# Kernel optimization log

Hardware: AMD Instinct MI355X
Metric: run time of the kernel (lower is better)

Reference implementation:

```python
import jax, jax.numpy as jnp
import numpy as np

D_MODEL = 1024
N_HEADS = 16
HEAD_DIM = D_MODEL // N_HEADS
SEQ = 2048
BATCH = 2
ROPE_BASE = 10000.0


def rope_cos_sin(seq_len, dim, dtype=jnp.float32):
    inv_freq = 1.0 / (ROPE_BASE ** (jnp.arange(0, dim, 2, dtype=jnp.float32) / dim))
    pos = jnp.arange(seq_len, dtype=jnp.float32)
    freqs = jnp.outer(pos, inv_freq)              # [S, dim/2]
    emb = jnp.concatenate([freqs, freqs], axis=-1)  # [S, dim]
    return jnp.cos(emb).astype(dtype), jnp.sin(emb).astype(dtype)


def rotate_half(x):
    x1, x2 = jnp.split(x, 2, axis=-1)
    return jnp.concatenate([-x2, x1], axis=-1)


def setup_inputs() -> dict:
    key = jax.random.key(0)
    kx, kq, kk, kv, ko = jax.random.split(key, 5)
    x = jax.random.normal(kx, (BATCH, SEQ, D_MODEL), dtype=jnp.float32)
    # causal boolean mask, broadcastable to [B, H, S, S]
    attn_mask = jnp.tril(jnp.ones((SEQ, SEQ), dtype=bool))[None, None]
    s = 1.0 / np.sqrt(D_MODEL)
    Wq = jax.random.normal(kq, (D_MODEL, D_MODEL), dtype=jnp.float32) * s
    Wk = jax.random.normal(kk, (D_MODEL, D_MODEL), dtype=jnp.float32) * s
    Wv = jax.random.normal(kv, (D_MODEL, D_MODEL), dtype=jnp.float32) * s
    Wo = jax.random.normal(ko, (D_MODEL, D_MODEL), dtype=jnp.float32) * s
    return {"x": x, "attn_mask": attn_mask, "Wq": Wq, "Wk": Wk, "Wv": Wv, "Wo": Wo}


def reference(x, attn_mask, Wq, Wk, Wv, Wo):
    B, S, _ = x.shape
    dtype = x.dtype
    # projections (nn.Linear: x @ W.T)
    def split_heads(t):
        return t.reshape(B, S, N_HEADS, HEAD_DIM).transpose(0, 2, 1, 3)  # [B,H,S,Dh]
    q = split_heads(x @ Wq.T)
    k = split_heads(x @ Wk.T)
    v = split_heads(x @ Wv.T)
    # RoPE
    cos, sin = rope_cos_sin(S, HEAD_DIM, dtype)  # [S, Dh]
    cos = cos[None, None]
    sin = sin[None, None]
    q = q * cos + rotate_half(q) * sin
    k = k * cos + rotate_half(k) * sin
    # float mask: 0 where True, finfo.min where False
    neg = jnp.finfo(dtype).min
    float_mask = jnp.where(attn_mask, jnp.zeros((), dtype), jnp.full((), neg, dtype))
    # scaled dot product attention
    scale = 1.0 / np.sqrt(HEAD_DIM)
    scores = jnp.einsum("bhqd,bhkd->bhqk", q, k) * scale + float_mask
    attn = jax.nn.softmax(scores, axis=-1)
    out = jnp.einsum("bhqk,bhkd->bhqd", attn, v)  # [B,H,S,Dh]
    out = out.transpose(0, 2, 1, 3).reshape(B, S, D_MODEL)
    return out @ Wo.T
```

## Files before the change

kernel.cpp:

```cpp
#include <hip/hip_runtime.h>
#include <hip/hip_bf16.h>
#include <math.h>

typedef unsigned short ushort_t;
typedef __attribute__((ext_vector_type(8))) short short8;
typedef __attribute__((ext_vector_type(4))) float f32x4;

#define D_MODEL 1024
#define SEQ     2048
#define NH      16
#define HD      64
#define BATCH   2
#define M_TOTAL (BATCH * SEQ)
#define SCL     0.18033688f
#define HSZ     4194304

__device__ __forceinline__ ushort_t f2bf(float f) {
    __hip_bfloat16 h = __float2bfloat16(f);
    ushort_t u;
    __builtin_memcpy(&u, &h, 2);
    return u;
}
__device__ __forceinline__ unsigned pack2(float a, float b) {
    __hip_bfloat162 h = __float22bfloat162_rn(make_float2(a, b));
    unsigned u;
    __builtin_memcpy(&u, &h, 4);
    return u;
}
__device__ __forceinline__ float fexp2(float x) { return __builtin_amdgcn_exp2f(x); }

typedef const __attribute__((address_space(1))) void* gp_t;
typedef __attribute__((address_space(3))) void* lp_t;
__device__ __forceinline__ void cp16(const void* g, void* l) {
    __builtin_amdgcn_global_load_lds((gp_t)g, (lp_t)l, 16, 0, 0);
}

__global__ __launch_bounds__(256) void prep(
    const float* __restrict__ x,
    const float* __restrict__ w0, const float* __restrict__ w1,
    const float* __restrict__ w2, const float* __restrict__ w3,
    ushort_t* __restrict__ xb, ushort_t* __restrict__ wb,
    float2* __restrict__ tab)
{
    int bid = blockIdx.x;
    if (bid < 4096) {
        size_t e = ((size_t)bid * 256 + threadIdx.x) * 8;
        const float* src;
        ushort_t* dst;
        size_t off;
        if (e < (size_t)HSZ) {
            src = x; dst = xb; off = e;
        } else {
            size_t r = e - HSZ;
            int j = (int)(r >> 20);
            off = r & 1048575u;
            src = (j == 0) ? w0 : (j == 1) ? w1 : (j == 2) ? w2 : w3;
            dst = wb + ((size_t)j << 20);
        }
        float4 a = *(const float4*)&src[off];
        float4 b = *(const float4*)&src[off + 4];
        uint4 u;
        u.x = pack2(a.x, a.y);
        u.y = pack2(a.z, a.w);
        u.z = pack2(b.x, b.y);
        u.w = pack2(b.z, b.w);
        *(uint4*)&dst[off] = u;
    } else {
        int idx = (bid - 4096) * 256 + threadIdx.x;
        int i = idx & 31, s = idx >> 5;
        float invf = powf(10000.0f, -(float)(2 * i) * (1.0f / 64.0f));
        float fr = (float)s * invf;
        float sn, cs;
        sincosf(fr, &sn, &cs);
        tab[idx] = make_float2(cs, sn);
    }
}


#define STAGE(K0, SB) do {                                                   \
    cp16(&A [(size_t)(m0 + ro0) * K + (K0) + c0 * 8], &As[SB][i0 * 8]);      \
    cp16(&A [(size_t)(m0 + ro1) * K + (K0) + c1 * 8], &As[SB][i1 * 8]);      \
    cp16(&Wp[(size_t)(n0 + ro0) * K + (K0) + c0 * 8], &Bs[SB][i0 * 8]);      \
    cp16(&Wp[(size_t)(n0 + ro1) * K + (K0) + c1 * 8], &Bs[SB][i1 * 8]);      \
} while (0)

#define K_ITER(SK0, BUF, SBUF, DOSTAGE, LAST) {                              \
    if constexpr (LAST) {                                                    \
        asm volatile("s_waitcnt vmcnt(0)" ::: "memory");                     \
    } else {                                                                 \
        asm volatile("s_waitcnt vmcnt(4)" ::: "memory");                     \
    }                                                                        \
    __builtin_amdgcn_s_barrier();                                            \
    if constexpr (DOSTAGE) { STAGE(SK0, SBUF); }                             \
    short8 af_[4], bf_[4];                                                   \
    _Pragma("unroll")                                                        \
    for (int i = 0; i < 4; ++i) {                                            \
        int R = wm + 16 * i + r15;                                           \
        af_[i] = *(const short8*)&As[BUF][(R * 4 + ((q4 + (R >> 1)) & 3)) * 8]; \
    }                                                                        \
    _Pragma("unroll")                                                        \
    for (int j = 0; j < 4; ++j) {                                            \
        int R = wn + 16 * j + r15;                                           \
        bf_[j] = *(const short8*)&Bs[BUF][(R * 4 + ((q4 + (R >> 1)) & 3)) * 8]; \
    }                                                                        \
    __builtin_amdgcn_s_setprio(1);                                           \
    _Pragma("unroll")                                                        \
    for (int i = 0; i < 4; ++i) {                                            \
        _Pragma("unroll")                                                    \
        for (int j = 0; j < 4; ++j)                                          \
            acc[i][j] = __builtin_amdgcn_mfma_f32_16x16x32_bf16(             \
                af_[i], bf_[j], acc[i][j], 0, 0, 0);                         \
    }                                                                        \
    __builtin_amdgcn_s_setprio(0);                                           \
    asm volatile("s_waitcnt lgkmcnt(0)" ::: "memory");                       \
    __builtin_amdgcn_s_barrier();                                            \
}

__global__ __launch_bounds__(256, 3) void gemm_qkv(
    const ushort_t* __restrict__ A,
    const ushort_t* __restrict__ W0, const ushort_t* __restrict__ W1,
    const ushort_t* __restrict__ W2,
    void* __restrict__ D0v, void* __restrict__ D1v, void* __restrict__ D2v,
    const float2* __restrict__ tab)
{
    __shared__ ushort_t As[3][128 * 32];
    __shared__ ushort_t Bs[3][128 * 32];
    const int K = D_MODEL;
    const int t = threadIdx.x;
    const int l = t & 63, w = t >> 6;
    const int wm = (w & 1) * 64, wn = (w >> 1) * 64;
    const int r15 = l & 15, q4 = l >> 4;

    const int bid = blockIdx.x;
    const int xcd = bid & 7, loc = bid >> 3;
    const int mt = (xcd >> 1) * 8 + (loc & 7);
    int rest = loc >> 3;
    const int nt = (xcd & 1) * 4 + (rest & 3);
    const int z  = rest >> 2;
    const int m0 = mt * 128, n0 = nt * 128;
    const ushort_t* Wp = (z == 0) ? W0 : (z == 1 ? W1 : W2);
    void* Dp           = (z == 0) ? D0v : (z == 1 ? D1v : D2v);

    f32x4 acc[4][4];
#pragma unroll
    for (int i = 0; i < 4; ++i)
#pragma unroll
        for (int j = 0; j < 4; ++j) acc[i][j] = (f32x4){0.f, 0.f, 0.f, 0.f};

    const int i0 = t, i1 = t + 256;
    const int ro0 = i0 >> 2, c0 = ((i0 & 3) - (ro0 >> 1)) & 3;
    const int ro1 = i1 >> 2, c1 = ((i1 & 3) - (ro1 >> 1)) & 3;

    STAGE(0, 0);
    STAGE(32, 1);
#pragma unroll 1
    for (int kb = 0; kb < 10; ++kb) {
        const int k6 = kb * 96;
        K_ITER(k6 + 64,  0, 2, 1, 0)
        K_ITER(k6 + 96,  1, 0, 1, 0)
        K_ITER(k6 + 128, 2, 1, 1, 0)
    }
    K_ITER(0, 0, 0, 0, 0)
    K_ITER(0, 1, 0, 0, 1)

    if (z < 2) {
        ushort_t* Dst = (ushort_t*)Dp;
        const float scl = (z == 0) ? SCL : 1.0f;
#pragma unroll
        for (int i = 0; i < 4; ++i) {
#pragma unroll
            for (int r = 0; r < 4; ++r) {
                int row = m0 + wm + 16 * i + q4 * 4 + r;
                int b = row >> 11, s = row & (SEQ - 1);
                const float2* trow = &tab[s * 32];
#pragma unroll
                for (int j = 0; j < 2; ++j) {
                    int col = n0 + wn + 16 * j + r15;
                    int h = col >> 6, f = 16 * j + r15;
                    float2 csn = trow[f];
                    float cs = csn.x * scl, sn = csn.y * scl;
                    float lo = acc[i][j][r], hi = acc[i][j + 2][r];
                    size_t o = (((size_t)(b * NH + h)) * SEQ + s) * HD + f;
                    Dst[o]      = f2bf(lo * cs - hi * sn);
                    Dst[o + 32] = f2bf(hi * cs + lo * sn);
                }
            }
        }
    } else {
        ushort_t* Dst = (ushort_t*)Dp;
#pragma unroll
        for (int i = 0; i < 4; ++i)
#pragma unroll
            for (int j = 0; j < 4; ++j) {
                int row0 = m0 + wm + 16 * i + q4 * 4;
                int col  = n0 + wn + 16 * j + r15;
                int b = row0 >> 11, s0 = row0 & (SEQ - 1);
                int h = col >> 6, d = col & (HD - 1);
                size_t o = (((size_t)(b * NH + h)) * HD + d) * SEQ + s0;
                uint2 u;
                u.x = pack2(acc[i][j][0], acc[i][j][1]);
                u.y = pack2(acc[i][j][2], acc[i][j][3]);
                *(uint2*)&Dst[o] = u;
            }
    }
}

#undef K_ITER
#undef STAGE


#define STAGE_O(K0, SB) do {                                                 \
    cp16(&A [(size_t)(m0 + roa0) * K + (K0) + ca0 * 8], &As[SB][ia0 * 8]);   \
    cp16(&A [(size_t)(m0 + roa1) * K + (K0) + ca1 * 8], &As[SB][ia1 * 8]);   \
    cp16(&A [(size_t)(m0 + roa2) * K + (K0) + ca2 * 8], &As[SB][ia2 * 8]);   \
    cp16(&A [(size_t)(m0 + roa3) * K + (K0) + ca3 * 8], &As[SB][ia3 * 8]);   \
    cp16(&Wp[(size_t)(n0 + rob0) * K + (K0) + cb0 * 8], &Bs[SB][ib0 * 8]);   \
    cp16(&Wp[(size_t)(n0 + rob1) * K + (K0) + cb1 * 8], &Bs[SB][ib1 * 8]);   \
} while (0)

#define K_ITER_O(SK0, BUF, SBUF, DOSTAGE, LAST) {                            \
    if constexpr (LAST) {                                                    \
        asm volatile("s_waitcnt vmcnt(0)" ::: "memory");                     \
    } else {                                                                 \
        asm volatile("s_waitcnt vmcnt(6)" ::: "memory");                     \
    }                                                                        \
    __builtin_amdgcn_s_barrier();                                            \
    if constexpr (DOSTAGE) { STAGE_O(SK0, SBUF); }                           \
    short8 af_[4][2], bf_[2][2];                                             \
    _Pragma("unroll")                                                        \
    for (int i = 0; i < 4; ++i) {                                            \
        int R = wm + 16 * i + r15;                                           \
        _Pragma("unroll")                                                    \
        for (int kk = 0; kk < 2; ++kk)                                       \
            af_[i][kk] = *(const short8*)                                    \
                &As[BUF][(R * 8 + ((kk * 4 + q4) ^ (R & 7))) * 8];           \
    }                                                                        \
    _Pragma("unroll")                                                        \
    for (int j = 0; j < 2; ++j) {                                            \
        int R = wn + 16 * j + r15;                                           \
        _Pragma("unroll")                                                    \
        for (int kk = 0; kk < 2; ++kk)                                       \
            bf_[j][kk] = *(const short8*)                                    \
                &Bs[BUF][(R * 8 + ((kk * 4 + q4) ^ (R & 7))) * 8];           \
    }                                                                        \
    __builtin_amdgcn_s_setprio(1);                                           \
    _Pragma("unroll")                                                        \
    for (int kk = 0; kk < 2; ++kk) {                                         \
        _Pragma("unroll")                                                    \
        for (int i = 0; i < 4; ++i) {                                        \
            _Pragma("unroll")                                                \
            for (int j = 0; j < 2; ++j)                                      \
                acc[i][j] = __builtin_amdgcn_mfma_f32_16x16x32_bf16(         \
                    af_[i][kk], bf_[j][kk], acc[i][j], 0, 0, 0);             \
        }                                                                    \
    }                                                                        \
    __builtin_amdgcn_s_setprio(0);                                           \
    asm volatile("s_waitcnt lgkmcnt(0)" ::: "memory");                       \
    __builtin_amdgcn_s_barrier();                                            \
}

__global__ __launch_bounds__(256, 2) void gemm_o(
    const ushort_t* __restrict__ A, const ushort_t* __restrict__ Wp,
    float* __restrict__ Dst)
{
    __shared__ ushort_t As[3][128 * 64];
    __shared__ ushort_t Bs[3][64 * 64];
    const int K = D_MODEL;
    const int t = threadIdx.x;
    const int l = t & 63, w = t >> 6;
    const int wm = (w & 1) * 64, wn = (w >> 1) * 32;
    const int r15 = l & 15, q4 = l >> 4;

    const int bid = blockIdx.x;
    const int xcd = bid & 7, loc = bid >> 3;
    const int mt = (xcd >> 1) * 8 + (loc & 7);
    const int nt = (xcd & 1) * 8 + (loc >> 3);
    const int m0 = mt * 128, n0 = nt * 64;

    f32x4 acc[4][2];
#pragma unroll
    for (int i = 0; i < 4; ++i)
#pragma unroll
        for (int j = 0; j < 2; ++j) acc[i][j] = (f32x4){0.f, 0.f, 0.f, 0.f};

    const int ia0 = t,       roa0 = ia0 >> 3, ca0 = (ia0 & 7) ^ (roa0 & 7);
    const int ia1 = t + 256, roa1 = ia1 >> 3, ca1 = (ia1 & 7) ^ (roa1 & 7);
    const int ia2 = t + 512, roa2 = ia2 >> 3, ca2 = (ia2 & 7) ^ (roa2 & 7);
    const int ia3 = t + 768, roa3 = ia3 >> 3, ca3 = (ia3 & 7) ^ (roa3 & 7);
    const int ib0 = t,       rob0 = ib0 >> 3, cb0 = (ib0 & 7) ^ (rob0 & 7);
    const int ib1 = t + 256, rob1 = ib1 >> 3, cb1 = (ib1 & 7) ^ (rob1 & 7);

    STAGE_O(0, 0);
    STAGE_O(64, 1);
#pragma unroll 1
    for (int kb = 0; kb < 4; ++kb) {
        const int k6 = kb * 192;
        K_ITER_O(k6 + 128, 0, 2, 1, 0)
        K_ITER_O(k6 + 192, 1, 0, 1, 0)
        K_ITER_O(k6 + 256, 2, 1, 1, 0)
    }
    K_ITER_O(896, 0, 2, 1, 0)
    K_ITER_O(960, 1, 0, 1, 0)
    K_ITER_O(0,   2, 0, 0, 0)
    K_ITER_O(0,   0, 0, 0, 1)

#pragma unroll
    for (int i = 0; i < 4; ++i)
#pragma unroll
        for (int j = 0; j < 2; ++j)
#pragma unroll
            for (int r = 0; r < 4; ++r) {
                int row = m0 + wm + 16 * i + q4 * 4 + r;
                int col = n0 + wn + 16 * j + r15;
                Dst[(size_t)row * D_MODEL + col] = acc[i][j][r];
            }
}

#undef K_ITER_O
#undef STAGE_O

__global__ __launch_bounds__(256, 3) void attn_fused(
    const ushort_t* __restrict__ Qw, const ushort_t* __restrict__ Kw,
    const ushort_t* __restrict__ Vt, ushort_t* __restrict__ Ow)
{
    __shared__ __align__(16) ushort_t Kl[2][64 * 64];
    __shared__ __align__(16) ushort_t Vl[2][64 * 64];
    __shared__ __align__(16) ushort_t Ps[4][16 * 72];

    const int t = threadIdx.x;
    const int l = t & 63, w = t >> 6;
    const int r15 = l & 15, q4 = l >> 4;
    const int bid = blockIdx.x;
    const int loc = bid >> 3;
    const int bh  = (bid & 7) * 4 + (loc & 3);
    const int s   = 31 - (loc >> 2);
    const int m   = s * 4 + w;
    const size_t baseQK = (size_t)bh * SEQ * HD;
    const size_t baseV  = (size_t)bh * HD * SEQ;

    const int L0 = t, L1 = t + 256;
    const int r0 = L0 >> 3, c0 = (L0 & 7) ^ (r0 & 7);
    const int r1 = L1 >> 3, c1 = (L1 & 7) ^ (r1 & 7);

    const ushort_t* qp = &Qw[baseQK + (size_t)(m * 16 + r15) * HD + q4 * 8];
    short8 qf0 = *(const short8*)qp;
    short8 qf1 = *(const short8*)(qp + 32);

    f32x4 oacc[4];
    float part[4];
#pragma unroll
    for (int nb = 0; nb < 4; ++nb) oacc[nb] = (f32x4){0.f, 0.f, 0.f, 0.f};
#pragma unroll
    for (int r = 0; r < 4; ++r) part[r] = 0.f;

    const int ig0 = m * 16 + q4 * 4;
    ushort_t* ps = &Ps[w][0];

    auto stage = [&](int jt, int buf) {
        cp16(&Kw[baseQK + (size_t)(jt * 64 + r0) * HD + c0 * 8], &Kl[buf][L0 * 8]);
        cp16(&Kw[baseQK + (size_t)(jt * 64 + r1) * HD + c1 * 8], &Kl[buf][L1 * 8]);
        cp16(&Vt[baseV + (size_t)r0 * SEQ + jt * 64 + c0 * 8],   &Vl[buf][L0 * 8]);
        cp16(&Vt[baseV + (size_t)r1 * SEQ + jt * 64 + c1 * 8],   &Vl[buf][L1 * 8]);
    };

    auto process = [&](int jt, int buf) {
        f32x4 sc[4];
        __builtin_amdgcn_s_setprio(1);
#pragma unroll
        for (int nb = 0; nb < 4; ++nb) {
            int R  = nb * 16 + r15;
            int a0 = R * 8 + (q4 ^ (R & 7));
            int a1 = R * 8 + ((q4 + 4) ^ (R & 7));
            short8 kb0 = *(const short8*)&Kl[buf][a0 * 8];
            short8 kb1 = *(const short8*)&Kl[buf][a1 * 8];
            f32x4 zz = (f32x4){0.f, 0.f, 0.f, 0.f};
            zz = __builtin_amdgcn_mfma_f32_16x16x32_bf16(qf0, kb0, zz, 0, 0, 0);
            sc[nb] = __builtin_amdgcn_mfma_f32_16x16x32_bf16(qf1, kb1, zz, 0, 0, 0);
        }
        __builtin_amdgcn_s_setprio(0);
        const bool diag = (jt == s);
#pragma unroll
        for (int r = 0; r < 4; ++r) {
            float p0 = fexp2(sc[0][r]), p1 = fexp2(sc[1][r]);
            float p2 = fexp2(sc[2][r]), p3 = fexp2(sc[3][r]);
            if (diag) {
                int qg = ig0 + r, jb = jt * 64 + r15;
                p0 = (jb      <= qg) ? p0 : 0.f;
                p1 = (jb + 16 <= qg) ? p1 : 0.f;
                p2 = (jb + 32 <= qg) ? p2 : 0.f;
                p3 = (jb + 48 <= qg) ? p3 : 0.f;
            }
            part[r] += (p0 + p1) + (p2 + p3);
            int ro = (q4 * 4 + r) * 72 + r15;
            ps[ro]      = f2bf(p0);
            ps[ro + 16] = f2bf(p1);
            ps[ro + 32] = f2bf(p2);
            ps[ro + 48] = f2bf(p3);
        }
        short8 pf0 = *(const short8*)&ps[r15 * 72 + q4 * 8];
        short8 pf1 = *(const short8*)&ps[r15 * 72 + q4 * 8 + 32];
        __builtin_amdgcn_s_setprio(1);
#pragma unroll
        for (int nb = 0; nb < 4; ++nb) {
            int R  = nb * 16 + r15;
            int a0 = R * 8 + (q4 ^ (R & 7));
            int a1 = R * 8 + ((q4 + 4) ^ (R & 7));
            short8 vb0 = *(const short8*)&Vl[buf][a0 * 8];
            short8 vb1 = *(const short8*)&Vl[buf][a1 * 8];
            f32x4 o = __builtin_amdgcn_mfma_f32_16x16x32_bf16(pf0, vb0, oacc[nb], 0, 0, 0);
            oacc[nb] = __builtin_amdgcn_mfma_f32_16x16x32_bf16(pf1, vb1, o, 0, 0, 0);
        }
        __builtin_amdgcn_s_setprio(0);
    };

    stage(0, 0);
    for (int jt = 0; jt <= s; ++jt) {
        __syncthreads();
        if (jt < s) stage(jt + 1, (jt + 1) & 1);
        process(jt, jt & 1);
    }

    float lsum[4];
#pragma unroll
    for (int r = 0; r < 4; ++r) {
        float rs = part[r];
#pragma unroll
        for (int off = 1; off < 16; off <<= 1)
            rs += __shfl_xor(rs, off, 64);
        lsum[r] = 1.0f / rs;
    }

    const int b = bh >> 4, h = bh & 15;
#pragma unroll
    for (int nb = 0; nb < 4; ++nb) {
#pragma unroll
        for (int r = 0; r < 4; ++r) {
            int sg = m * 16 + q4 * 4 + r;
            int d  = nb * 16 + r15;
            Ow[((size_t)(b * SEQ + sg)) * D_MODEL + h * HD + d] =
                f2bf(oacc[nb][r] * lsum[r]);
        }
    }
}

extern "C" void kernel_launch(void* const* d_in, const int* in_sizes, int n_in,
                              void* d_out, int out_size, void* d_ws, size_t ws_size,
                              hipStream_t stream)
{
    const float* x  = (const float*)d_in[0];
    const float* Wq = (const float*)d_in[2];
    const float* Wk = (const float*)d_in[3];
    const float* Wv = (const float*)d_in[4];
    const float* Wo = (const float*)d_in[5];

    ushort_t* qw = (ushort_t*)d_ws;
    ushort_t* kw = qw + HSZ;
    ushort_t* vt = kw + HSZ;
    ushort_t* xb = vt + HSZ;
    ushort_t* aw = xb;
    ushort_t* wb = xb + HSZ;
    float2*  tab = (float2*)(wb + HSZ);

    prep<<<4096 + 256, 256, 0, stream>>>(x, Wq, Wk, Wv, Wo, xb, wb, tab);
    gemm_qkv<<<768, 256, 0, stream>>>(
        xb, wb, wb + (1 << 20), wb + (2 << 20), qw, kw, vt, tab);
    attn_fused<<<1024, 256, 0, stream>>>(qw, kw, vt, aw);
    gemm_o<<<512, 256, 0, stream>>>(aw, wb + (3 << 20), (float*)d_out);
}
```

Baseline: 177.6 us.

## Enlarge attention query tile to 128 rows with paired causal block scheduling

Each attention block now handles 128 query rows instead of 64: every wave computes two 16-row sub-tiles, so each staged K/V tile in LDS feeds twice as many MFMAs. Blocks are paired light/heavy (T and 15-T) within each XCD so the causal workload is balanced, and the grid is halved to 512. Waves skip processing tiles beyond their own diagonal but still take part in staging. The setprio hints are removed and launch bounds drop to 2 blocks per CU to make room for the doubled accumulators, which lowers occupancy.

```diff
diff --git a/kernel.cpp b/kernel.cpp
--- a/kernel.cpp
+++ b/kernel.cpp
@@ -319,22 +319,27 @@
 #undef K_ITER_O
 #undef STAGE_O
 
-__global__ __launch_bounds__(256, 3) void attn_fused(
+__global__ __launch_bounds__(256, 2) void attn_fused(
     const ushort_t* __restrict__ Qw, const ushort_t* __restrict__ Kw,
     const ushort_t* __restrict__ Vt, ushort_t* __restrict__ Ow)
 {
     __shared__ __align__(16) ushort_t Kl[2][64 * 64];
     __shared__ __align__(16) ushort_t Vl[2][64 * 64];
-    __shared__ __align__(16) ushort_t Ps[4][16 * 72];
+    __shared__ __align__(16) ushort_t Ps[4][32 * 72];
 
     const int t = threadIdx.x;
     const int l = t & 63, w = t >> 6;
     const int r15 = l & 15, q4 = l >> 4;
     const int bid = blockIdx.x;
-    const int loc = bid >> 3;
-    const int bh  = (bid & 7) * 4 + (loc & 3);
-    const int s   = 31 - (loc >> 2);
-    const int m   = s * 4 + w;
+    const int xcd = bid & 7, loc = bid >> 3;
+    const int p   = loc >> 1, e = loc & 1;
+    const int head_l = p >> 3, u = p & 7;
+    const int T   = e ? u : (15 - u);
+    const int bh  = xcd * 4 + head_l;
+    const int B0  = T * 128;
+    const int NT  = 2 * T + 2;
+    const int rb0 = B0 + 32 * w;
+    const int wtop = rb0 >> 6;
     const size_t baseQK = (size_t)bh * SEQ * HD;
     const size_t baseV  = (size_t)bh * HD * SEQ;
 
@@ -342,18 +347,25 @@
     const int r0 = L0 >> 3, c0 = (L0 & 7) ^ (r0 & 7);
     const int r1 = L1 >> 3, c1 = (L1 & 7) ^ (r1 & 7);
 
-    const ushort_t* qp = &Qw[baseQK + (size_t)(m * 16 + r15) * HD + q4 * 8];
-    short8 qf0 = *(const short8*)qp;
-    short8 qf1 = *(const short8*)(qp + 32);
-
-    f32x4 oacc[4];
-    float part[4];
-#pragma unroll
-    for (int nb = 0; nb < 4; ++nb) oacc[nb] = (f32x4){0.f, 0.f, 0.f, 0.f};
-#pragma unroll
-    for (int r = 0; r < 4; ++r) part[r] = 0.f;
-
-    const int ig0 = m * 16 + q4 * 4;
+    short8 qf[2][2];
+#pragma unroll
+    for (int s = 0; s < 2; ++s) {
+        const ushort_t* qp =
+            &Qw[baseQK + (size_t)(rb0 + 16 * s + r15) * HD + q4 * 8];
+        qf[s][0] = *(const short8*)qp;
+        qf[s][1] = *(const short8*)(qp + 32);
+    }
+
+    f32x4 oacc[2][4];
+    float part[2][4];
+#pragma unroll
+    for (int s = 0; s < 2; ++s)
+#pragma unroll
+        for (int nb = 0; nb < 4; ++nb) {
+            oacc[s][nb] = (f32x4){0.f, 0.f, 0.f, 0.f};
+            part[s][nb] = 0.f;
+        }
+
     ushort_t* ps = &Ps[w][0];
 
     auto stage = [&](int jt, int buf) {
@@ -364,8 +376,7 @@
     };
 
     auto process = [&](int jt, int buf) {
-        f32x4 sc[4];
-        __builtin_amdgcn_s_setprio(1);
+        f32x4 sc[2][4];
 #pragma unroll
         for (int nb = 0; nb < 4; ++nb) {
             int R  = nb * 16 + r15;
@@ -373,33 +384,42 @@
             int a1 = R * 8 + ((q4 + 4) ^ (R & 7));
             short8 kb0 = *(const short8*)&Kl[buf][a0 * 8];
             short8 kb1 = *(const short8*)&Kl[buf][a1 * 8];
-            f32x4 zz = (f32x4){0.f, 0.f, 0.f, 0.f};
-            zz = __builtin_amdgcn_mfma_f32_16x16x32_bf16(qf0, kb0, zz, 0, 0, 0);
-            sc[nb] = __builtin_amdgcn_mfma_f32_16x16x32_bf16(qf1, kb1, zz, 0, 0, 0);
-        }
-        __builtin_amdgcn_s_setprio(0);
-        const bool diag = (jt == s);
-#pragma unroll
-        for (int r = 0; r < 4; ++r) {
-            float p0 = fexp2(sc[0][r]), p1 = fexp2(sc[1][r]);
-            float p2 = fexp2(sc[2][r]), p3 = fexp2(sc[3][r]);
-            if (diag) {
-                int qg = ig0 + r, jb = jt * 64 + r15;
-                p0 = (jb      <= qg) ? p0 : 0.f;
-                p1 = (jb + 16 <= qg) ? p1 : 0.f;
-                p2 = (jb + 32 <= qg) ? p2 : 0.f;
-                p3 = (jb + 48 <= qg) ? p3 : 0.f;
-            }
-            part[r] += (p0 + p1) + (p2 + p3);
-            int ro = (q4 * 4 + r) * 72 + r15;
-            ps[ro]      = f2bf(p0);
-            ps[ro + 16] = f2bf(p1);
-            ps[ro + 32] = f2bf(p2);
-            ps[ro + 48] = f2bf(p3);
-        }
-        short8 pf0 = *(const short8*)&ps[r15 * 72 + q4 * 8];
-        short8 pf1 = *(const short8*)&ps[r15 * 72 + q4 * 8 + 32];
-        __builtin_amdgcn_s_setprio(1);
+#pragma unroll
+            for (int s = 0; s < 2; ++s) {
+                f32x4 zz = (f32x4){0.f, 0.f, 0.f, 0.f};
+                zz = __builtin_amdgcn_mfma_f32_16x16x32_bf16(qf[s][0], kb0, zz, 0, 0, 0);
+                sc[s][nb] = __builtin_amdgcn_mfma_f32_16x16x32_bf16(qf[s][1], kb1, zz, 0, 0, 0);
+            }
+        }
+        const bool diag = (jt == wtop);
+#pragma unroll
+        for (int s = 0; s < 2; ++s) {
+            const int ig0 = rb0 + 16 * s + q4 * 4;
+#pragma unroll
+            for (int r = 0; r < 4; ++r) {
+                float p0 = fexp2(sc[s][0][r]), p1 = fexp2(sc[s][1][r]);
+                float p2 = fexp2(sc[s][2][r]), p3 = fexp2(sc[s][3][r]);
+                if (diag) {
+                    int qg = ig0 + r, jb = jt * 64 + r15;
+                    p0 = (jb      <= qg) ? p0 : 0.f;
+                    p1 = (jb + 16 <= qg) ? p1 : 0.f;
+                    p2 = (jb + 32 <= qg) ? p2 : 0.f;
+                    p3 = (jb + 48 <= qg) ? p3 : 0.f;
+                }
+                part[s][r] += (p0 + p1) + (p2 + p3);
+                int ro = (s * 16 + q4 * 4 + r) * 72 + r15;
+                ps[ro]      = f2bf(p0);
+                ps[ro + 16] = f2bf(p1);
+                ps[ro + 32] = f2bf(p2);
+                ps[ro + 48] = f2bf(p3);
+            }
+        }
+        short8 pf[2][2];
+#pragma unroll
+        for (int s = 0; s < 2; ++s) {
+            pf[s][0] = *(const short8*)&ps[(s * 16 + r15) * 72 + q4 * 8];
+            pf[s][1] = *(const short8*)&ps[(s * 16 + r15) * 72 + q4 * 8 + 32];
+        }
 #pragma unroll
         for (int nb = 0; nb < 4; ++nb) {
             int R  = nb * 16 + r15;
@@ -407,38 +427,42 @@
             int a1 = R * 8 + ((q4 + 4) ^ (R & 7));
             short8 vb0 = *(const short8*)&Vl[buf][a0 * 8];
             short8 vb1 = *(const short8*)&Vl[buf][a1 * 8];
-            f32x4 o = __builtin_amdgcn_mfma_f32_16x16x32_bf16(pf0, vb0, oacc[nb], 0, 0, 0);
-            oacc[nb] = __builtin_amdgcn_mfma_f32_16x16x32_bf16(pf1, vb1, o, 0, 0, 0);
-        }
-        __builtin_amdgcn_s_setprio(0);
+#pragma unroll
+            for (int s = 0; s < 2; ++s) {
+                f32x4 o = __builtin_amdgcn_mfma_f32_16x16x32_bf16(pf[s][0], vb0, oacc[s][nb], 0, 0, 0);
+                oacc[s][nb] = __builtin_amdgcn_mfma_f32_16x16x32_bf16(pf[s][1], vb1, o, 0, 0, 0);
+            }
+        }
     };
 
     stage(0, 0);
-    for (int jt = 0; jt <= s; ++jt) {
+    for (int jt = 0; jt < NT; ++jt) {
         __syncthreads();
-        if (jt < s) stage(jt + 1, (jt + 1) & 1);
-        process(jt, jt & 1);
-    }
-
-    float lsum[4];
-#pragma unroll
-    for (int r = 0; r < 4; ++r) {
-        float rs = part[r];
-#pragma unroll
-        for (int off = 1; off < 16; off <<= 1)
-            rs += __shfl_xor(rs, off, 64);
-        lsum[r] = 1.0f / rs;
+        if (jt < NT - 1) stage(jt + 1, (jt + 1) & 1);
+        if (jt <= wtop) process(jt, jt & 1);
     }
 
     const int b = bh >> 4, h = bh & 15;
 #pragma unroll
-    for (int nb = 0; nb < 4; ++nb) {
+    for (int s = 0; s < 2; ++s) {
+        float lsum[4];
 #pragma unroll
         for (int r = 0; r < 4; ++r) {
-            int sg = m * 16 + q4 * 4 + r;
-            int d  = nb * 16 + r15;
-            Ow[((size_t)(b * SEQ + sg)) * D_MODEL + h * HD + d] =
-                f2bf(oacc[nb][r] * lsum[r]);
+            float rs = part[s][r];
+#pragma unroll
+            for (int off = 1; off < 16; off <<= 1)
+                rs += __shfl_xor(rs, off, 64);
+            lsum[r] = 1.0f / rs;
+        }
+#pragma unroll
+        for (int nb = 0; nb < 4; ++nb) {
+#pragma unroll
+            for (int r = 0; r < 4; ++r) {
+                int sg = rb0 + 16 * s + q4 * 4 + r;
+                int d  = nb * 16 + r15;
+                Ow[((size_t)(b * SEQ + sg)) * D_MODEL + h * HD + d] =
+                    f2bf(oacc[s][nb][r] * lsum[r]);
+            }
         }
     }
 }
@@ -464,6 +488,6 @@
     prep<<<4096 + 256, 256, 0, stream>>>(x, Wq, Wk, Wv, Wo, xb, wb, tab);
     gemm_qkv<<<768, 256, 0, stream>>>(
         xb, wb, wb + (1 << 20), wb + (2 << 20), qw, kw, vt, tab);
-    attn_fused<<<1024, 256, 0, stream>>>(qw, kw, vt, aw);
+    attn_fused<<<512, 256, 0, stream>>>(qw, kw, vt, aw);
     gemm_o<<<512, 256, 0, stream>>>(aw, wb + (3 << 20), (float*)d_out);
 }
```

Measured after the change: 201.5 us. 13.4% more time.
